# Performance work log

Hardware: AMD Instinct MI355X
Metric: run time of the kernel (lower is better)

Reference implementation:

```python
import jax, jax.numpy as jnp
import numpy as np

B, N, C = 4, 2048, 768
H = 12
HD = C // H  # 64
SCALE = HD ** -0.5


def setup_inputs() -> dict:
    key = jax.random.key(0)
    ks = jax.random.split(key, 3)
    x = jax.random.normal(ks[0], (B, N, C), dtype=jnp.float32)
    w_qkv = jax.random.normal(ks[1], (C, 3 * C), dtype=jnp.float32) * (C ** -0.5)
    b_qkv = jnp.zeros((3 * C,), dtype=jnp.float32)
    w_proj = jax.random.normal(ks[2], (C, C), dtype=jnp.float32) * (C ** -0.5)
    b_proj = jnp.zeros((C,), dtype=jnp.float32)
    return {"x": x, "w_qkv": w_qkv, "b_qkv": b_qkv, "w_proj": w_proj, "b_proj": b_proj}


def reference(x, w_qkv, b_qkv, w_proj, b_proj):
    # fused QKV projection: [B, N, 3C] -> [3, B, H, N, HD]
    qkv = (x @ w_qkv + b_qkv).reshape(B, N, 3, H, HD).transpose(2, 0, 3, 1, 4)
    q, k, v = qkv[0] * SCALE, qkv[1], qkv[2]
    # scores [B, H, N, N] (Global mixer: no mask)
    attn = jnp.einsum('bhnd,bhmd->bhnm', q, k)
    attn = jax.nn.softmax(attn, axis=-1)
    # attn @ V -> [B, N, C]
    out = jnp.einsum('bhnm,bhmd->bhnd', attn, v).transpose(0, 2, 1, 3).reshape(B, N, C)
    return out @ w_proj + b_proj
```

## Files before the change

kernel.cpp:

```cpp
#include <hip/hip_runtime.h>
#include <hip/hip_bf16.h>
#include <math.h>

#define B_ 4
#define N_ 2048
#define C_ 768
#define H_ 12
#define HD_ 64

typedef short short8 __attribute__((ext_vector_type(8)));
typedef float float16v __attribute__((ext_vector_type(16)));
typedef unsigned short u16;
typedef unsigned int u32;

static __device__ __forceinline__ u16 f2bf(float x) {
    __hip_bfloat16 b = __float2bfloat16(x);
    return *reinterpret_cast<u16*>(&b);
}
static __device__ __forceinline__ u32 pack2(float lo, float hi) {
    return (u32)f2bf(lo) | ((u32)f2bf(hi) << 16);
}
static __device__ __forceinline__ u32 rne2(float lo, float hi) {
    u32 a = __builtin_bit_cast(u32, lo);
    u32 b = __builtin_bit_cast(u32, hi);
    a = a + 0x7fffu + ((a >> 16) & 1u);
    b = b + 0x7fffu + ((b >> 16) & 1u);
    return (a >> 16) | (b & 0xffff0000u);
}
static __device__ __forceinline__ void gload_lds16(const u16* g, u16* l) {
    __builtin_amdgcn_global_load_lds(
        (const __attribute__((address_space(1))) void*)g,
        (__attribute__((address_space(3))) void*)l, 16, 0, 0);
}

__global__ __launch_bounds__(256) void cast_bf16_kernel(
    const float* __restrict__ X, u16* __restrict__ Xb, int n4)
{
    int i = blockIdx.x * 256 + threadIdx.x;
    if (i < n4) {
        float4 v = ((const float4*)X)[i];
        uint2 o = make_uint2(pack2(v.x, v.y), pack2(v.z, v.w));
        ((uint2*)Xb)[i] = o;
    }
}

__global__ __launch_bounds__(256) void transpose_cvt_kernel(
    const float* __restrict__ W, u16* __restrict__ Wt, int R, int Cc)
{
    __shared__ float tile[64][65];
    const int t = threadIdx.x;
    const int r0 = blockIdx.y * 64, c0 = blockIdx.x * 64;
    const int tr = t >> 4, tc = (t & 15) * 4;
#pragma unroll
    for (int i = 0; i < 4; i++) {
        float4 v = *(const float4*)(W + (size_t)(r0 + tr + i * 16) * Cc + c0 + tc);
        tile[tr + i * 16][tc + 0] = v.x;
        tile[tr + i * 16][tc + 1] = v.y;
        tile[tr + i * 16][tc + 2] = v.z;
        tile[tr + i * 16][tc + 3] = v.w;
    }
    __syncthreads();
#pragma unroll
    for (int i = 0; i < 4; i++) {
        int n = tr + i * 16;
        int k = tc;
        uint2 o = make_uint2(pack2(tile[k + 0][n], tile[k + 1][n]),
                             pack2(tile[k + 2][n], tile[k + 3][n]));
        *(uint2*)(Wt + (size_t)(c0 + n) * R + r0 + k) = o;
    }
}

template<bool OUT_BF16>
__global__ __launch_bounds__(256) void gemm_mfma_kernel(
    const u16* __restrict__ A, int lda,
    const u16* __restrict__ Bt,
    const float* __restrict__ bias,
    void* __restrict__ C, int ldc,
    int K, float scale, int scale_cols)
{
    __shared__ u16 As[128 * 64];
    __shared__ u16 Bs[128 * 64];
    const int t = threadIdx.x;
    const int w = t >> 6, lane = t & 63, ln = lane & 31, e = lane >> 5;
    const int wm = w >> 1, wn = w & 1;
    const int row0 = blockIdx.y * 128, col0 = blockIdx.x * 128;
    const int r_sub = lane >> 3;
    const int cg = (lane & 7) ^ r_sub;

    float16v acc[2][2];
#pragma unroll
    for (int i = 0; i < 16; i++) {
        acc[0][0][i] = 0.f; acc[0][1][i] = 0.f;
        acc[1][0][i] = 0.f; acc[1][1][i] = 0.f;
    }

    for (int k0 = 0; k0 < K; k0 += 64) {
        __syncthreads();
#pragma unroll
        for (int i = 0; i < 4; i++) {
            int rr = w * 32 + i * 8;
            const u16* ga = A + (size_t)(row0 + rr + r_sub) * lda + k0 + cg * 8;
            gload_lds16(ga, As + rr * 64);
            const u16* gb = Bt + (size_t)(col0 + rr + r_sub) * K + k0 + cg * 8;
            gload_lds16(gb, Bs + rr * 64);
        }
        __syncthreads();

#pragma unroll
        for (int ks = 0; ks < 4; ks++) {
            short8 af[2], bf[2];
#pragma unroll
            for (int sm = 0; sm < 2; sm++) {
                int r = wm * 64 + sm * 32 + ln;
                af[sm] = *(const short8*)&As[r * 64 + ((2 * ks + e) ^ (r & 7)) * 8];
            }
#pragma unroll
            for (int sn = 0; sn < 2; sn++) {
                int r = wn * 64 + sn * 32 + ln;
                bf[sn] = *(const short8*)&Bs[r * 64 + ((2 * ks + e) ^ (r & 7)) * 8];
            }
#pragma unroll
            for (int sm = 0; sm < 2; sm++)
#pragma unroll
                for (int sn = 0; sn < 2; sn++)
                    acc[sm][sn] = __builtin_amdgcn_mfma_f32_32x32x16_bf16(
                        af[sm], bf[sn], acc[sm][sn], 0, 0, 0);
        }
    }

    const float sc = (col0 < scale_cols) ? scale : 1.0f;
#pragma unroll
    for (int sm = 0; sm < 2; sm++)
#pragma unroll
        for (int sn = 0; sn < 2; sn++) {
            int col = col0 + wn * 64 + sn * 32 + ln;
            float bv = bias[col];
#pragma unroll
            for (int reg = 0; reg < 16; reg++) {
                int row = row0 + wm * 64 + sm * 32 + (reg & 3) + 8 * (reg >> 2) + 4 * e;
                float v = (acc[sm][sn][reg] + bv) * sc;
                if (OUT_BF16)
                    ((u16*)C)[(size_t)row * ldc + col] = f2bf(v);
                else
                    ((float*)C)[(size_t)row * ldc + col] = v;
            }
        }
}

__global__ __launch_bounds__(256) void attn_kernel(u16* __restrict__ qkvb)
{
    __shared__ __align__(16) u16 lds_us[17408];
    u16* Ks = lds_us;
    u32* VtU = (u32*)(lds_us + 4096);

    const int t = threadIdx.x;
    const int w = t >> 6, lane = t & 63, ln = lane & 31, e = lane >> 5;
    const int r_sub = lane >> 3;
    const int cgk = (lane & 7) ^ r_sub;
    const int bh = blockIdx.y;
    const int b = bh / H_, h = bh % H_;
    const int row0 = blockIdx.x * 128;
    const size_t base = (size_t)b * N_ * 2304 + h * 64;

    short8 qf[4];
    {
        const u16* qrow = qkvb + base + (size_t)(row0 + w * 32 + ln) * 2304;
#pragma unroll
        for (int ks = 0; ks < 4; ks++)
            qf[ks] = __builtin_bit_cast(short8, *(const uint4*)(qrow + ks * 16 + e * 8));
    }
    const int kp = t >> 3, g = t & 7;
    const int vcol = ((kp >> 2) ^ g) * 4 + (kp & 3);

    float16v accO0, accO1;
#pragma unroll
    for (int i = 0; i < 16; i++) { accO0[i] = 0.f; accO1[i] = 0.f; }
    float l = 0.f;
    const float L2E = 1.4426950408889634f;
    const float MB = 8.0f * L2E;

    for (int kc = 0; kc < N_; kc += 64) {
        __syncthreads();
#pragma unroll
        for (int i = 0; i < 2; i++) {
            int rbase = w * 16 + i * 8;
            const u16* gk = qkvb + base + (size_t)(kc + rbase + r_sub) * 2304 + 768 + cgk * 8;
            gload_lds16(gk, Ks + rbase * 64);
        }
        {
            const u16* gv = qkvb + base + (size_t)(kc + 2 * kp) * 2304 + 1536 + g * 8;
            uint4 va4 = *(const uint4*)gv;
            uint4 vb4 = *(const uint4*)(gv + 2304);
            const u16* va = (const u16*)&va4;
            const u16* vb = (const u16*)&vb4;
#pragma unroll
            for (int j = 0; j < 8; j++)
                VtU[(g * 8 + j) * 36 + vcol] = (u32)va[j] | ((u32)vb[j] << 16);
        }
        __syncthreads();

        float16v s0, s1;
#pragma unroll
        for (int i = 0; i < 16; i++) { s0[i] = 0.f; s1[i] = 0.f; }
#pragma unroll
        for (int ks = 0; ks < 4; ks++) {
            int slot = (2 * ks + e) ^ (ln & 7);
            short8 k0 = *(const short8*)&Ks[ln * 64 + slot * 8];
            short8 k1 = *(const short8*)&Ks[(32 + ln) * 64 + slot * 8];
            s0 = __builtin_amdgcn_mfma_f32_32x32x16_bf16(k0, qf[ks], s0, 0, 0, 0);
            s1 = __builtin_amdgcn_mfma_f32_32x32x16_bf16(k1, qf[ks], s1, 0, 0, 0);
        }

        float t0[16], t1[16];
#pragma unroll
        for (int i = 0; i < 16; i++) {
            t0[i] = exp2f(fmaf(s0[i], L2E, -MB));
            t1[i] = exp2f(fmaf(s1[i], L2E, -MB));
            s0[i] = t0[i]; s1[i] = t1[i];
        }
#pragma unroll
        for (int i = 0; i < 8; i++) { t0[i] += t0[i + 8]; t1[i] += t1[i + 8]; }
#pragma unroll
        for (int i = 0; i < 4; i++) { t0[i] += t0[i + 4]; t1[i] += t1[i + 4]; }
        float lsum = ((t0[0] + t0[1]) + (t0[2] + t0[3])) +
                     ((t1[0] + t1[1]) + (t1[2] + t1[3]));
        lsum += __shfl_xor(lsum, 32);
        l += lsum;

#pragma unroll
        for (int kk = 0; kk < 4; kk++) {
            const int mloc = kk & 1;
            float p0, p1, p2, p3, p4, p5, p6, p7;
            if (kk < 2) {
                p0 = s0[8 * mloc + 0]; p1 = s0[8 * mloc + 1]; p2 = s0[8 * mloc + 2]; p3 = s0[8 * mloc + 3];
                p4 = s0[8 * mloc + 4]; p5 = s0[8 * mloc + 5]; p6 = s0[8 * mloc + 6]; p7 = s0[8 * mloc + 7];
            } else {
                p0 = s1[8 * mloc + 0]; p1 = s1[8 * mloc + 1]; p2 = s1[8 * mloc + 2]; p3 = s1[8 * mloc + 3];
                p4 = s1[8 * mloc + 4]; p5 = s1[8 * mloc + 5]; p6 = s1[8 * mloc + 6]; p7 = s1[8 * mloc + 7];
            }
            u32 L01 = rne2(p0, p1), L23 = rne2(p2, p3);
            u32 H01 = rne2(p4, p5), H23 = rne2(p6, p7);
            u32 sL01 = (u32)__shfl_xor((int)L01, 32);
            u32 sL23 = (u32)__shfl_xor((int)L23, 32);
            u32 sH01 = (u32)__shfl_xor((int)H01, 32);
            u32 sH23 = (u32)__shfl_xor((int)H23, 32);
            uint4 pf4 = make_uint4(e ? sH01 : L01, e ? sH23 : L23,
                                   e ? H01 : sL01, e ? H23 : sL23);
            short8 pfrag = __builtin_bit_cast(short8, pf4);

            int blk = kk * 2 + e;
            uint4 v0 = *(const uint4*)&VtU[ln * 36 + (blk ^ (ln >> 3)) * 4];
            uint4 v1 = *(const uint4*)&VtU[(ln + 32) * 36 + (blk ^ ((ln + 32) >> 3)) * 4];
            short8 va0 = __builtin_bit_cast(short8, v0);
            short8 va1 = __builtin_bit_cast(short8, v1);
            accO0 = __builtin_amdgcn_mfma_f32_32x32x16_bf16(va0, pfrag, accO0, 0, 0, 0);
            accO1 = __builtin_amdgcn_mfma_f32_32x32x16_bf16(va1, pfrag, accO1, 0, 0, 0);
        }
    }

    __syncthreads();
    float* Os = (float*)lds_us + w * (32 * 68);
    float linv = 1.0f / l;
#pragma unroll
    for (int reg = 0; reg < 16; reg++) {
        int d = (reg & 3) + 8 * (reg >> 2) + 4 * e;
        Os[ln * 68 + d] = accO0[reg] * linv;
        Os[ln * 68 + d + 32] = accO1[reg] * linv;
    }
#pragma unroll
    for (int j = 0; j < 4; j++) {
        int idx = lane + j * 64;
        int r = idx >> 3, gg = idx & 7;
        float4 o0 = *(float4*)&Os[r * 68 + gg * 8];
        float4 o1 = *(float4*)&Os[r * 68 + gg * 8 + 4];
        uint4 ov = make_uint4(pack2(o0.x, o0.y), pack2(o0.z, o0.w),
                              pack2(o1.x, o1.y), pack2(o1.z, o1.w));
        *(uint4*)(qkvb + base + (size_t)(row0 + w * 32 + r) * 2304 + gg * 8) = ov;
    }
}

extern "C" void kernel_launch(void* const* d_in, const int* in_sizes, int n_in,
                              void* d_out, int out_size, void* d_ws, size_t ws_size,
                              hipStream_t stream) {
    const float* x      = (const float*)d_in[0];
    const float* w_qkv  = (const float*)d_in[1];
    const float* b_qkv  = (const float*)d_in[2];
    const float* w_proj = (const float*)d_in[3];
    const float* b_proj = (const float*)d_in[4];
    float* out = (float*)d_out;

    char* ws = (char*)d_ws;
    u16* qkvb   = (u16*)ws;
    u16* xb     = (u16*)(ws + 37748736);
    u16* wqkvT  = (u16*)(ws + 50331648);
    u16* wprojT = (u16*)(ws + 53870592);

    cast_bf16_kernel<<<6144, 256, 0, stream>>>(x, xb, (B_ * N_ * C_) / 4);
    transpose_cvt_kernel<<<dim3(36, 12), 256, 0, stream>>>(w_qkv, wqkvT, C_, 3 * C_);
    transpose_cvt_kernel<<<dim3(12, 12), 256, 0, stream>>>(w_proj, wprojT, C_, C_);

    gemm_mfma_kernel<true><<<dim3(18, 64), 256, 0, stream>>>(
        xb, C_, wqkvT, b_qkv, qkvb, 3 * C_, C_, 0.125f, C_);

    attn_kernel<<<dim3(16, 48), 256, 0, stream>>>(qkvb);

    gemm_mfma_kernel<false><<<dim3(6, 64), 256, 0, stream>>>(
        qkvb, 3 * C_, wprojT, b_proj, out, C_, C_, 1.0f, 0);
}
```

Baseline: 253.7 us.

## Produce transposed V via separate GEMM and load it directly into LDS

The QKV projection is split in two. One GEMM writes Q and K into a packed buffer. A second GEMM computes V transposed (W_v^T · x^T, with the bias applied per row) straight into a [C, B*N] layout. The attention kernel can then fetch V tiles with async global-to-LDS loads and a swizzled layout, replacing the per-iteration register transpose and scattered LDS stores. The output goes to a separate buffer for the projection GEMM. The change also swaps the float-to-bf16 packing for a hardware packed-convert builtin when it is available. The cost is an extra GEMM launch, and the transposed-output GEMM has strided row-wise bias reads and column-scattered stores.

Result: slower. 261.3 us (+3.0%).

```diff
diff --git a/kernel.cpp b/kernel.cpp
--- a/kernel.cpp
+++ b/kernel.cpp
@@ -16,9 +16,6 @@
 static __device__ __forceinline__ u16 f2bf(float x) {
     __hip_bfloat16 b = __float2bfloat16(x);
     return *reinterpret_cast<u16*>(&b);
-}
-static __device__ __forceinline__ u32 pack2(float lo, float hi) {
-    return (u32)f2bf(lo) | ((u32)f2bf(hi) << 16);
 }
 static __device__ __forceinline__ u32 rne2(float lo, float hi) {
     u32 a = __builtin_bit_cast(u32, lo);
@@ -27,6 +24,18 @@
     b = b + 0x7fffu + ((b >> 16) & 1u);
     return (a >> 16) | (b & 0xffff0000u);
 }
+#if defined(__has_builtin)
+#if __has_builtin(__builtin_amdgcn_cvt_pk_bf16_f32)
+#define HAVE_CVT_PK_BF16 1
+#endif
+#endif
+static __device__ __forceinline__ u32 cpk(float lo, float hi) {
+#ifdef HAVE_CVT_PK_BF16
+    return __builtin_bit_cast(u32, __builtin_amdgcn_cvt_pk_bf16_f32(lo, hi));
+#else
+    return rne2(lo, hi);
+#endif
+}
 static __device__ __forceinline__ void gload_lds16(const u16* g, u16* l) {
     __builtin_amdgcn_global_load_lds(
         (const __attribute__((address_space(1))) void*)g,
@@ -39,7 +48,7 @@
     int i = blockIdx.x * 256 + threadIdx.x;
     if (i < n4) {
         float4 v = ((const float4*)X)[i];
-        uint2 o = make_uint2(pack2(v.x, v.y), pack2(v.z, v.w));
+        uint2 o = make_uint2(cpk(v.x, v.y), cpk(v.z, v.w));
         ((uint2*)Xb)[i] = o;
     }
 }
@@ -64,13 +73,13 @@
     for (int i = 0; i < 4; i++) {
         int n = tr + i * 16;
         int k = tc;
-        uint2 o = make_uint2(pack2(tile[k + 0][n], tile[k + 1][n]),
-                             pack2(tile[k + 2][n], tile[k + 3][n]));
+        uint2 o = make_uint2(cpk(tile[k + 0][n], tile[k + 1][n]),
+                             cpk(tile[k + 2][n], tile[k + 3][n]));
         *(uint2*)(Wt + (size_t)(c0 + n) * R + r0 + k) = o;
     }
 }
 
-template<bool OUT_BF16>
+template<bool OUT_BF16, bool BIAS_ROW>
 __global__ __launch_bounds__(256) void gemm_mfma_kernel(
     const u16* __restrict__ A, int lda,
     const u16* __restrict__ Bt,
@@ -134,10 +143,11 @@
 #pragma unroll
         for (int sn = 0; sn < 2; sn++) {
             int col = col0 + wn * 64 + sn * 32 + ln;
-            float bv = bias[col];
+            float bvc = BIAS_ROW ? 0.f : bias[col];
 #pragma unroll
             for (int reg = 0; reg < 16; reg++) {
                 int row = row0 + wm * 64 + sm * 32 + (reg & 3) + 8 * (reg >> 2) + 4 * e;
+                float bv = BIAS_ROW ? bias[row] : bvc;
                 float v = (acc[sm][sn][reg] + bv) * sc;
                 if (OUT_BF16)
                     ((u16*)C)[(size_t)row * ldc + col] = f2bf(v);
@@ -147,11 +157,12 @@
         }
 }
 
-__global__ __launch_bounds__(256) void attn_kernel(u16* __restrict__ qkvb)
+__global__ __launch_bounds__(256) void attn_kernel(
+    const u16* __restrict__ qk, const u16* __restrict__ Vt, u16* __restrict__ Ob)
 {
     __shared__ __align__(16) u16 lds_us[17408];
     u16* Ks = lds_us;
-    u32* VtU = (u32*)(lds_us + 4096);
+    u16* Vs = lds_us + 4096;
 
     const int t = threadIdx.x;
     const int w = t >> 6, lane = t & 63, ln = lane & 31, e = lane >> 5;
@@ -160,17 +171,14 @@
     const int bh = blockIdx.y;
     const int b = bh / H_, h = bh % H_;
     const int row0 = blockIdx.x * 128;
-    const size_t base = (size_t)b * N_ * 2304 + h * 64;
 
     short8 qf[4];
     {
-        const u16* qrow = qkvb + base + (size_t)(row0 + w * 32 + ln) * 2304;
+        const u16* qrow = qk + (size_t)(b * N_ + row0 + w * 32 + ln) * 1536 + h * 64;
 #pragma unroll
         for (int ks = 0; ks < 4; ks++)
             qf[ks] = __builtin_bit_cast(short8, *(const uint4*)(qrow + ks * 16 + e * 8));
     }
-    const int kp = t >> 3, g = t & 7;
-    const int vcol = ((kp >> 2) ^ g) * 4 + (kp & 3);
 
     float16v accO0, accO1;
 #pragma unroll
@@ -184,18 +192,12 @@
 #pragma unroll
         for (int i = 0; i < 2; i++) {
             int rbase = w * 16 + i * 8;
-            const u16* gk = qkvb + base + (size_t)(kc + rbase + r_sub) * 2304 + 768 + cgk * 8;
+            const u16* gk = qk + (size_t)(b * N_ + kc + rbase + r_sub) * 1536
+                               + 768 + h * 64 + cgk * 8;
             gload_lds16(gk, Ks + rbase * 64);
-        }
-        {
-            const u16* gv = qkvb + base + (size_t)(kc + 2 * kp) * 2304 + 1536 + g * 8;
-            uint4 va4 = *(const uint4*)gv;
-            uint4 vb4 = *(const uint4*)(gv + 2304);
-            const u16* va = (const u16*)&va4;
-            const u16* vb = (const u16*)&vb4;
-#pragma unroll
-            for (int j = 0; j < 8; j++)
-                VtU[(g * 8 + j) * 36 + vcol] = (u32)va[j] | ((u32)vb[j] << 16);
+            const u16* gv = Vt + (size_t)(h * 64 + rbase + r_sub) * (B_ * N_)
+                               + b * N_ + kc + cgk * 8;
+            gload_lds16(gv, Vs + rbase * 64);
         }
         __syncthreads();
 
@@ -238,8 +240,8 @@
                 p0 = s1[8 * mloc + 0]; p1 = s1[8 * mloc + 1]; p2 = s1[8 * mloc + 2]; p3 = s1[8 * mloc + 3];
                 p4 = s1[8 * mloc + 4]; p5 = s1[8 * mloc + 5]; p6 = s1[8 * mloc + 6]; p7 = s1[8 * mloc + 7];
             }
-            u32 L01 = rne2(p0, p1), L23 = rne2(p2, p3);
-            u32 H01 = rne2(p4, p5), H23 = rne2(p6, p7);
+            u32 L01 = cpk(p0, p1), L23 = cpk(p2, p3);
+            u32 H01 = cpk(p4, p5), H23 = cpk(p6, p7);
             u32 sL01 = (u32)__shfl_xor((int)L01, 32);
             u32 sL23 = (u32)__shfl_xor((int)L23, 32);
             u32 sH01 = (u32)__shfl_xor((int)H01, 32);
@@ -248,11 +250,9 @@
                                    e ? H01 : sL01, e ? H23 : sL23);
             short8 pfrag = __builtin_bit_cast(short8, pf4);
 
-            int blk = kk * 2 + e;
-            uint4 v0 = *(const uint4*)&VtU[ln * 36 + (blk ^ (ln >> 3)) * 4];
-            uint4 v1 = *(const uint4*)&VtU[(ln + 32) * 36 + (blk ^ ((ln + 32) >> 3)) * 4];
-            short8 va0 = __builtin_bit_cast(short8, v0);
-            short8 va1 = __builtin_bit_cast(short8, v1);
+            int slot = (2 * kk + e) ^ (ln & 7);
+            short8 va0 = *(const short8*)&Vs[ln * 64 + slot * 8];
+            short8 va1 = *(const short8*)&Vs[(32 + ln) * 64 + slot * 8];
             accO0 = __builtin_amdgcn_mfma_f32_32x32x16_bf16(va0, pfrag, accO0, 0, 0, 0);
             accO1 = __builtin_amdgcn_mfma_f32_32x32x16_bf16(va1, pfrag, accO1, 0, 0, 0);
         }
@@ -273,9 +273,9 @@
         int r = idx >> 3, gg = idx & 7;
         float4 o0 = *(float4*)&Os[r * 68 + gg * 8];
         float4 o1 = *(float4*)&Os[r * 68 + gg * 8 + 4];
-        uint4 ov = make_uint4(pack2(o0.x, o0.y), pack2(o0.z, o0.w),
-                              pack2(o1.x, o1.y), pack2(o1.z, o1.w));
-        *(uint4*)(qkvb + base + (size_t)(row0 + w * 32 + r) * 2304 + gg * 8) = ov;
+        uint4 ov = make_uint4(cpk(o0.x, o0.y), cpk(o0.z, o0.w),
+                              cpk(o1.x, o1.y), cpk(o1.z, o1.w));
+        *(uint4*)(Ob + (size_t)(b * N_ + row0 + w * 32 + r) * 768 + h * 64 + gg * 8) = ov;
     }
 }
 
@@ -290,20 +290,25 @@
     float* out = (float*)d_out;
 
     char* ws = (char*)d_ws;
-    u16* qkvb   = (u16*)ws;
-    u16* xb     = (u16*)(ws + 37748736);
-    u16* wqkvT  = (u16*)(ws + 50331648);
-    u16* wprojT = (u16*)(ws + 53870592);
+    u16* qk2    = (u16*)ws;
+    u16* Vt     = (u16*)(ws + 25165824);
+    u16* Ob     = (u16*)(ws + 37748736);
+    u16* xb     = (u16*)(ws + 50331648);
+    u16* wqkvT  = (u16*)(ws + 62914560);
+    u16* wprojT = (u16*)(ws + 66453504);
 
     cast_bf16_kernel<<<6144, 256, 0, stream>>>(x, xb, (B_ * N_ * C_) / 4);
     transpose_cvt_kernel<<<dim3(36, 12), 256, 0, stream>>>(w_qkv, wqkvT, C_, 3 * C_);
     transpose_cvt_kernel<<<dim3(12, 12), 256, 0, stream>>>(w_proj, wprojT, C_, C_);
 
-    gemm_mfma_kernel<true><<<dim3(18, 64), 256, 0, stream>>>(
-        xb, C_, wqkvT, b_qkv, qkvb, 3 * C_, C_, 0.125f, C_);
-
-    attn_kernel<<<dim3(16, 48), 256, 0, stream>>>(qkvb);
-
-    gemm_mfma_kernel<false><<<dim3(6, 64), 256, 0, stream>>>(
-        qkvb, 3 * C_, wprojT, b_proj, out, C_, C_, 1.0f, 0);
-}
+    gemm_mfma_kernel<true, false><<<dim3(12, 64), 256, 0, stream>>>(
+        xb, C_, wqkvT, b_qkv, qk2, 1536, C_, 0.125f, 768);
+
+    gemm_mfma_kernel<true, true><<<dim3(64, 6), 256, 0, stream>>>(
+        wqkvT + (size_t)1536 * C_, C_, xb, b_qkv + 1536, Vt, B_ * N_, C_, 1.0f, 0);
+
+    attn_kernel<<<dim3(16, 48), 256, 0, stream>>>(qk2, Vt, Ob);
+
+    gemm_mfma_kernel<false, false><<<dim3(6, 64), 256, 0, stream>>>(
+        Ob, C_, wprojT, b_proj, out, C_, C_, 1.0f, 0);
+}
```
